# Optimization experiments

Measured on AMD Instinct MI355X. Metric: run time of the kernel, lower is better.

Reference implementation:

```python
import jax, jax.numpy as jnp
import numpy as np

B, LENGTH, D, IN = 32, 32, 384, 384
NCELLS = LENGTH * (LENGTH + 1) // 2  # 528

def _offsets():
    off = np.zeros(LENGTH, dtype=np.int64)
    for lvl in range(1, LENGTH):
        off[lvl] = off[lvl - 1] + (LENGTH - (lvl - 1))
    return off

_OFF = _offsets()

def _inside_index(level):
    Ls = LENGTH - level
    pos = np.arange(Ls)[:, None]
    k = np.arange(level)[None, :]
    left = _OFF[k] + pos                      # span (k, pos)
    right = _OFF[level - k - 1] + pos + k + 1  # span (level-k-1, pos+k+1)
    return jnp.asarray(left), jnp.asarray(right)

def _outside_index(level):
    Ls = LENGTH - level
    N = LENGTH - level - 1  # constant #contexts per position
    par = np.zeros((Ls, N), dtype=np.int64)
    sib = np.zeros((Ls, N), dtype=np.int64)
    for pos in range(Ls):
        j = 0
        for s in range(LENGTH - pos - level - 1):  # node is left child
            par[pos, j] = _OFF[level + s + 1] + pos
            sib[pos, j] = _OFF[s] + pos + level + 1
            j += 1
        for s in range(pos):  # node is right child
            par[pos, j] = _OFF[level + s + 1] + pos - s - 1
            sib[pos, j] = _OFF[s] + pos - s - 1
            j += 1
    return jnp.asarray(par), jnp.asarray(sib)

def sigma_h(x):
    return x * jnp.tanh(jnp.sqrt(jax.nn.sigmoid(x)))

def layer_norm(x, g, b, eps=1e-5):
    mu = x.mean(-1, keepdims=True)
    var = ((x - mu) ** 2).mean(-1, keepdims=True)
    return (x - mu) * jax.lax.rsqrt(var + eps) * g + b

def compose(l, r, W0, W1, B0, W2, B1):
    h = sigma_h(l @ W0 + r @ W1 + B0)
    return sigma_h(h @ W2 + B1)

def bilinear(u, v, M):
    return jnp.einsum('blnd,de,blne->bln', u, M, v)[..., None]

def setup_inputs() -> dict:
    key = jax.random.key(0)
    ks = jax.random.split(key, 16)
    sc = 1.0 / np.sqrt(D)
    mk = lambda k, shp: (jax.random.normal(k, shp, dtype=jnp.float32) * sc)
    inp = {
        'x': jax.random.normal(ks[0], (B, LENGTH, IN), dtype=jnp.float32),
        'leaf_W': mk(ks[1], (IN, D)), 'leaf_b': jnp.zeros((D,), jnp.float32),
        'in_ln_g': jnp.ones((D,), jnp.float32), 'in_ln_b': jnp.zeros((D,), jnp.float32),
        'out_ln_g': jnp.ones((D,), jnp.float32), 'out_ln_b': jnp.zeros((D,), jnp.float32),
        'root_h': jax.random.normal(ks[2], (D,), dtype=jnp.float32) * 0.02,
        'in_bi': mk(ks[3], (D, D)), 'out_bi': mk(ks[4], (D, D)),
        'in_W0': mk(ks[5], (D, D)), 'in_W1': mk(ks[6], (D, D)),
        'in_B0': jnp.zeros((D,), jnp.float32),
        'in_W2': mk(ks[7], (D, D)), 'in_B1': jnp.zeros((D,), jnp.float32),
        'out_W0': mk(ks[8], (D, D)), 'out_W1': mk(ks[9], (D, D)),
        'out_B0': jnp.zeros((D,), jnp.float32),
        'out_W2': mk(ks[10], (D, D)), 'out_B1': jnp.zeros((D,), jnp.float32),
    }
    return inp

def reference(x, leaf_W, leaf_b, in_ln_g, in_ln_b, out_ln_g, out_ln_b, root_h,
              in_bi, out_bi, in_W0, in_W1, in_B0, in_W2, in_B1,
              out_W0, out_W1, out_B0, out_W2, out_B1):
    # leaf transform
    h0 = layer_norm(sigma_h(x @ leaf_W + leaf_b), in_ln_g, in_ln_b)
    ih = jnp.zeros((B, NCELLS, D), x.dtype).at[:, :LENGTH].set(h0)
    is_ = jnp.zeros((B, NCELLS, 1), x.dtype)
    # inside pass (CKY chart, level-by-level)
    for level in range(1, LENGTH):
        li, ri = _inside_index(level)
        lh, rh = ih[:, li], ih[:, ri]   # [B, Ls, level, D]
        ls, rs = is_[:, li], is_[:, ri]
        sc = bilinear(lh, rh, in_bi) + ls + rs
        p = jax.nn.softmax(sc, axis=2)
        xc = compose(lh, rh, in_W0, in_W1, in_B0, in_W2, in_B1)
        hbar = layer_norm((p * xc).sum(2), in_ln_g, in_ln_b)
        sbar = (p * sc).sum(2)
        o = int(_OFF[level]); Ls = LENGTH - level
        ih = ih.at[:, o:o + Ls].set(hbar)
        is_ = is_.at[:, o:o + Ls].set(sbar)
    # outside pass
    oh = jnp.zeros((B, NCELLS, D), x.dtype)
    os_ = jnp.zeros((B, NCELLS, 1), x.dtype)
    root = layer_norm(jnp.broadcast_to(root_h, (B, 1, D)), out_ln_g, out_ln_b)
    oh = oh.at[:, -1:].set(root)
    for level in range(LENGTH - 2, -1, -1):
        pi, si = _outside_index(level)
        ph, sh = oh[:, pi], ih[:, si]   # parent outside / sibling inside
        ps, ss = os_[:, pi], is_[:, si]
        sc = bilinear(sh, ph, out_bi) + ss + ps
        p = jax.nn.softmax(sc, axis=2)
        xc = compose(ph, sh, out_W0, out_W1, out_B0, out_W2, out_B1)
        hbar = layer_norm((p * xc).sum(2), out_ln_g, out_ln_b)
        sbar = (p * sc).sum(2)
        o = int(_OFF[level]); Ls = LENGTH - level
        oh = oh.at[:, o:o + Ls].set(hbar)
        os_ = os_.at[:, o:o + Ls].set(sbar)
    return ih, is_, oh, os_
```

## Files before the change

### kernel.cpp

```cpp
#include <hip/hip_runtime.h>
#include <cstddef>

#define BDIM 32
#define LEN 32
#define DD 384
#define NCELLS 528

typedef _Float16 h16;
typedef __attribute__((ext_vector_type(8))) _Float16 v8h;
typedef __attribute__((ext_vector_type(4))) float v4f;

__device__ __forceinline__ int offf(int k) { return k * 32 - ((k * (k - 1)) >> 1); }
static inline int offh(int k) { return k * 32 - ((k * (k - 1)) >> 1); }

__device__ __forceinline__ float sigma_h_f(float x) {
  float s = 1.0f / (1.0f + __expf(-x));
  float r = sqrtf(s);
  float e2 = __expf(2.0f * r);
  float th = 1.0f - 2.0f / (e2 + 1.0f);
  return x * th;
}

__device__ __forceinline__ size_t rowbase(int r, int gLs, int gOff) {
  if (gLs == 0) return (size_t)r;
  int b = r / gLs;
  int p = r - b * gLs;
  return (size_t)b * NCELLS + gOff + p;
}

__device__ __forceinline__ void split16(float v, h16& h, h16& l) {
  h = (h16)v;
  l = (h16)(v - (float)h);
}

__global__ __launch_bounds__(256) void pack3_k(
    const float* __restrict__ w0, const float* __restrict__ w1,
    const float* __restrict__ bi, const float* __restrict__ ow1,
    const float* __restrict__ obi, const float* __restrict__ w2,
    const float* __restrict__ ow2, const float* __restrict__ ow0,
    const float* __restrict__ lw, const float* __restrict__ x,
    h16* __restrict__ WCth, h16* __restrict__ WCtl,
    h16* __restrict__ W2th, h16* __restrict__ W2tl,
    h16* __restrict__ OW2th, h16* __restrict__ OW2tl,
    h16* __restrict__ OW0th, h16* __restrict__ OW0tl,
    h16* __restrict__ LWth, h16* __restrict__ LWtl,
    h16* __restrict__ xh, h16* __restrict__ xl,
    float* __restrict__ isp, float* __restrict__ osp) {
  int i = blockIdx.x * 256 + threadIdx.x;
  if (i < 1920 * 384) {
    int n = i / 384, k = i - n * 384;
    int sel = n / 384, c = n - sel * 384;
    const float* src = sel == 0 ? w0 : sel == 1 ? w1 : sel == 2 ? bi
                       : sel == 3 ? ow1 : obi;
    float v = src[k * 384 + c];
    h16 h, l; split16(v, h, l);
    WCth[i] = h; WCtl[i] = l;
  }
  if (i < 384 * 384) {
    int n = i / 384, k = i - n * 384;
    h16 h, l;
    split16(w2[k * 384 + n], h, l);  W2th[i] = h;  W2tl[i] = l;
    split16(ow2[k * 384 + n], h, l); OW2th[i] = h; OW2tl[i] = l;
    split16(ow0[k * 384 + n], h, l); OW0th[i] = h; OW0tl[i] = l;
    split16(lw[k * 384 + n], h, l);  LWth[i] = h;  LWtl[i] = l;
  }
  if (i < 1024 * 384) {
    h16 h, l; split16(x[i], h, l);
    xh[i] = h; xl[i] = l;
  }
  if (i < BDIM * NCELLS) { isp[i] = 0.0f; osp[i] = 0.0f; }
}

__global__ __launch_bounds__(256) void gemmh(
    const h16* __restrict__ Ahp, const h16* __restrict__ Alp,
    const h16* __restrict__ Bth, const h16* __restrict__ Btl,
    const float* __restrict__ bias, float* __restrict__ C,
    int M, int N, int act, int gLs, int gOff) {
  __shared__ h16 Ah[64][40], Al[64][40];
  __shared__ h16 Bh[128][40], Bl[128][40];
  int tid = threadIdx.x;
  int w = tid >> 6, lane = tid & 63;
  int m0 = blockIdx.x * 64, n0 = blockIdx.y * 128;
  int r = lane & 15, q = lane >> 4;

  v4f acc[4][2];
#pragma unroll
  for (int i = 0; i < 4; ++i)
#pragma unroll
    for (int j = 0; j < 2; ++j) acc[i][j] = (v4f){0.f, 0.f, 0.f, 0.f};

  int sar = tid >> 2;
  int sak = (tid & 3) << 3;
  const h16* Aph = nullptr;
  const h16* Apl = nullptr;
  if (m0 + sar < M) {
    size_t rb = (size_t)(m0 + sar) * DD;
    Aph = Ahp + rb + sak;
    Apl = Alp + rb + sak;
  }
  int sbc = tid >> 1;
  int sbk = (tid & 1) << 4;
  const h16* Bph = Bth + (size_t)(n0 + sbc) * DD + sbk;
  const h16* Bpl = Btl + (size_t)(n0 + sbc) * DD + sbk;

  for (int k0 = 0; k0 < DD; k0 += 32) {
    v8h a_h = (v8h){0.f, 0.f, 0.f, 0.f, 0.f, 0.f, 0.f, 0.f};
    v8h a_l = a_h;
    if (Aph) {
      a_h = *reinterpret_cast<const v8h*>(Aph + k0);
      a_l = *reinterpret_cast<const v8h*>(Apl + k0);
    }
    v8h b_h0 = *reinterpret_cast<const v8h*>(Bph + k0);
    v8h b_h1 = *reinterpret_cast<const v8h*>(Bph + k0 + 8);
    v8h b_l0 = *reinterpret_cast<const v8h*>(Bpl + k0);
    v8h b_l1 = *reinterpret_cast<const v8h*>(Bpl + k0 + 8);
    __syncthreads();
    *reinterpret_cast<v8h*>(&Ah[sar][sak]) = a_h;
    *reinterpret_cast<v8h*>(&Al[sar][sak]) = a_l;
    *reinterpret_cast<v8h*>(&Bh[sbc][sbk]) = b_h0;
    *reinterpret_cast<v8h*>(&Bh[sbc][sbk + 8]) = b_h1;
    *reinterpret_cast<v8h*>(&Bl[sbc][sbk]) = b_l0;
    *reinterpret_cast<v8h*>(&Bl[sbc][sbk + 8]) = b_l1;
    __syncthreads();
    v8h afh[4], afl[4], bfh[2], bfl[2];
#pragma unroll
    for (int i = 0; i < 4; ++i) {
      afh[i] = *reinterpret_cast<const v8h*>(&Ah[i * 16 + r][q * 8]);
      afl[i] = *reinterpret_cast<const v8h*>(&Al[i * 16 + r][q * 8]);
    }
#pragma unroll
    for (int j = 0; j < 2; ++j) {
      bfh[j] = *reinterpret_cast<const v8h*>(&Bh[w * 32 + j * 16 + r][q * 8]);
      bfl[j] = *reinterpret_cast<const v8h*>(&Bl[w * 32 + j * 16 + r][q * 8]);
    }
#pragma unroll
    for (int i = 0; i < 4; ++i)
#pragma unroll
      for (int j = 0; j < 2; ++j) {
        acc[i][j] = __builtin_amdgcn_mfma_f32_16x16x32_f16(afl[i], bfh[j], acc[i][j], 0, 0, 0);
        acc[i][j] = __builtin_amdgcn_mfma_f32_16x16x32_f16(afh[i], bfl[j], acc[i][j], 0, 0, 0);
        acc[i][j] = __builtin_amdgcn_mfma_f32_16x16x32_f16(afh[i], bfh[j], acc[i][j], 0, 0, 0);
      }
  }

#pragma unroll
  for (int i = 0; i < 4; ++i) {
#pragma unroll
    for (int reg = 0; reg < 4; ++reg) {
      int rr = m0 + i * 16 + q * 4 + reg;
      if (rr >= M) continue;
      size_t cb = rowbase(rr, gLs, gOff) * (size_t)N;
#pragma unroll
      for (int j = 0; j < 2; ++j) {
        int col = n0 + w * 32 + j * 16 + r;
        float v = acc[i][j][reg];
        if (bias) v += bias[col];
        if (act) v = sigma_h_f(v);
        C[cb + col] = v;
      }
    }
  }
}

__global__ __launch_bounds__(256) void k1_in(
    const float* __restrict__ PC, const float* __restrict__ ihp,
    float* __restrict__ isp, h16* __restrict__ Hh, h16* __restrict__ Hl,
    float* __restrict__ Pw, const float* __restrict__ B0,
    int L, int Ls, int offL) {
  int g = blockIdx.x;
  int b = g / Ls, pos = g - b * Ls;
  int tid = threadIdx.x, lane = tid & 63, wv = tid >> 6;
  __shared__ float scs[32];
  size_t cb = (size_t)b * NCELLS;
  for (int n = wv; n < L; n += 4) {
    int lc = offf(n) + pos;
    int rc = offf(L - 1 - n) + pos + n + 1;
    const float* u = PC + (cb + lc) * 1920 + 768;
    const float* v = ihp + (cb + rc) * (size_t)DD;
    float s = 0.0f;
#pragma unroll
    for (int jj = 0; jj < 6; ++jj) s += u[lane + 64 * jj] * v[lane + 64 * jj];
#pragma unroll
    for (int o = 32; o; o >>= 1) s += __shfl_xor(s, o, 64);
    if (lane == 0) scs[n] = s + isp[cb + lc] + isp[cb + rc];
  }
  __syncthreads();
  if (wv == 0) {
    float v = (lane < L) ? scs[lane] : -3.0e38f;
    float m = v;
#pragma unroll
    for (int o = 32; o; o >>= 1) m = fmaxf(m, __shfl_xor(m, o, 64));
    float e = (lane < L) ? __expf(v - m) : 0.0f;
    float S = e;
#pragma unroll
    for (int o = 32; o; o >>= 1) S += __shfl_xor(S, o, 64);
    float pn = e / S;
    if (lane < L) Pw[(size_t)g * L + lane] = pn;
    float sb = (lane < L) ? pn * v : 0.0f;
#pragma unroll
    for (int o = 32; o; o >>= 1) sb += __shfl_xor(sb, o, 64);
    if (lane == 0) isp[cb + offL + pos] = sb;
  }
  for (int n = 0; n < L; ++n) {
    int lc = offf(n) + pos;
    int rc = offf(L - 1 - n) + pos + n + 1;
    const float* A0r = PC + (cb + lc) * 1920;
    const float* A1r = PC + (cb + rc) * 1920 + 384;
    size_t hb = ((size_t)g * L + n) * DD;
    for (int k = tid; k < DD; k += 256) {
      float v = sigma_h_f(A0r[k] + A1r[k] + B0[k]);
      h16 h = (h16)v;
      Hh[hb + k] = h;
      Hl[hb + k] = (h16)(v - (float)h);
    }
  }
}

__global__ __launch_bounds__(256) void k1_out(
    const float* __restrict__ PC, const float* __restrict__ P0,
    const float* __restrict__ ohp, const float* __restrict__ isp,
    float* __restrict__ osp, h16* __restrict__ Hh, h16* __restrict__ Hl,
    float* __restrict__ Pw, const float* __restrict__ B0,
    int L, int Ls, int Nc, int offL) {
  int g = blockIdx.x;
  int b = g / Ls, pos = g - b * Ls;
  int tid = threadIdx.x, lane = tid & 63, wv = tid >> 6;
  __shared__ float scs[32];
  size_t cb = (size_t)b * NCELLS;
  int cnt0 = 31 - pos - L;
  for (int j = wv; j < Nc; j += 4) {
    int par, sib;
    if (j < cnt0) { par = offf(L + j + 1) + pos; sib = offf(j) + pos + L + 1; }
    else { int s2 = j - cnt0; par = offf(L + s2 + 1) + pos - s2 - 1; sib = offf(s2) + pos - s2 - 1; }
    const float* u = PC + (cb + sib) * 1920 + 1536;
    const float* v = ohp + (cb + par) * (size_t)DD;
    float s = 0.0f;
#pragma unroll
    for (int jj = 0; jj < 6; ++jj) s += u[lane + 64 * jj] * v[lane + 64 * jj];
#pragma unroll
    for (int o = 32; o; o >>= 1) s += __shfl_xor(s, o, 64);
    if (lane == 0) scs[j] = s + isp[cb + sib] + osp[cb + par];
  }
  __syncthreads();
  if (wv == 0) {
    float v = (lane < Nc) ? scs[lane] : -3.0e38f;
    float m = v;
#pragma unroll
    for (int o = 32; o; o >>= 1) m = fmaxf(m, __shfl_xor(m, o, 64));
    float e = (lane < Nc) ? __expf(v - m) : 0.0f;
    float S = e;
#pragma unroll
    for (int o = 32; o; o >>= 1) S += __shfl_xor(S, o, 64);
    float pn = e / S;
    if (lane < Nc) Pw[(size_t)g * Nc + lane] = pn;
    float sb = (lane < Nc) ? pn * v : 0.0f;
#pragma unroll
    for (int o = 32; o; o >>= 1) sb += __shfl_xor(sb, o, 64);
    if (lane == 0) osp[cb + offL + pos] = sb;
  }
  for (int j = 0; j < Nc; ++j) {
    int par, sib;
    if (j < cnt0) { par = offf(L + j + 1) + pos; sib = offf(j) + pos + L + 1; }
    else { int s2 = j - cnt0; par = offf(L + s2 + 1) + pos - s2 - 1; sib = offf(s2) + pos - s2 - 1; }
    const float* p0r = P0 + (cb + par) * (size_t)DD;
    const float* s1r = PC + (cb + sib) * 1920 + 1152;
    size_t hb = ((size_t)g * Nc + j) * DD;
    for (int k = tid; k < DD; k += 256) {
      float v = sigma_h_f(p0r[k] + s1r[k] + B0[k]);
      h16 h = (h16)v;
      Hh[hb + k] = h;
      Hl[hb + k] = (h16)(v - (float)h);
    }
  }
}

__global__ __launch_bounds__(128) void k3_red_ln(
    const float* __restrict__ XC, const float* __restrict__ Pw,
    const float* __restrict__ lng, const float* __restrict__ lnb,
    float* __restrict__ outArr, h16* __restrict__ outh, h16* __restrict__ outl,
    int L, int Ls, int offL) {
  int g = blockIdx.x;
  int b = g / Ls, pos = g - b * Ls;
  int tid = threadIdx.x;
  float a0 = 0, a1 = 0, a2 = 0;
  const float* base = XC + (size_t)g * L * DD;
  for (int n = 0; n < L; ++n) {
    float pw = Pw ? Pw[(size_t)g * L + n] : 1.0f;
    const float* row = base + (size_t)n * DD;
    a0 += pw * row[tid];
    a1 += pw * row[tid + 128];
    a2 += pw * row[tid + 256];
  }
  int lane = tid & 63, wv = tid >> 6;
  float s = a0 + a1 + a2;
#pragma unroll
  for (int o = 32; o; o >>= 1) s += __shfl_xor(s, o, 64);
  __shared__ float r1[2], r2[2];
  if (lane == 0) r1[wv] = s;
  __syncthreads();
  float mean = (r1[0] + r1[1]) * (1.0f / 384.0f);
  float d0 = a0 - mean, d1 = a1 - mean, d2 = a2 - mean;
  float q = d0 * d0 + d1 * d1 + d2 * d2;
#pragma unroll
  for (int o = 32; o; o >>= 1) q += __shfl_xor(q, o, 64);
  if (lane == 0) r2[wv] = q;
  __syncthreads();
  float var = (r2[0] + r2[1]) * (1.0f / 384.0f);
  float inv = rsqrtf(var + 1e-5f);
  size_t ob = ((size_t)b * NCELLS + offL + pos) * DD;
  float* out = outArr + ob;
  float v0 = d0 * inv * lng[tid]       + lnb[tid];
  float v1 = d1 * inv * lng[tid + 128] + lnb[tid + 128];
  float v2 = d2 * inv * lng[tid + 256] + lnb[tid + 256];
  out[tid]       = v0;
  out[tid + 128] = v1;
  out[tid + 256] = v2;
  size_t sb = (size_t)g * DD;
  h16 h;
  h = (h16)v0; outh[sb + tid]       = h; outl[sb + tid]       = (h16)(v0 - (float)h);
  h = (h16)v1; outh[sb + tid + 128] = h; outl[sb + tid + 128] = (h16)(v1 - (float)h);
  h = (h16)v2; outh[sb + tid + 256] = h; outl[sb + tid + 256] = (h16)(v2 - (float)h);
}

__global__ __launch_bounds__(384) void root_k(
    const float* __restrict__ rooth, const float* __restrict__ lng,
    const float* __restrict__ lnb, const float* __restrict__ W0,
    float* __restrict__ ohp, float* __restrict__ P0) {
  int tid = threadIdx.x;
  int lane = tid & 63, wv = tid >> 6;
  __shared__ float rl[384];
  __shared__ float r1[6], r2[6];
  float x = rooth[tid];
  float s = x;
#pragma unroll
  for (int o = 32; o; o >>= 1) s += __shfl_xor(s, o, 64);
  if (lane == 0) r1[wv] = s;
  __syncthreads();
  float mean = (r1[0] + r1[1] + r1[2] + r1[3] + r1[4] + r1[5]) * (1.0f / 384.0f);
  float d = x - mean;
  float q = d * d;
#pragma unroll
  for (int o = 32; o; o >>= 1) q += __shfl_xor(q, o, 64);
  if (lane == 0) r2[wv] = q;
  __syncthreads();
  float var = (r2[0] + r2[1] + r2[2] + r2[3] + r2[4] + r2[5]) * (1.0f / 384.0f);
  float inv = rsqrtf(var + 1e-5f);
  float v = d * inv * lng[tid] + lnb[tid];
  rl[tid] = v;
  __syncthreads();
  for (int b2 = 0; b2 < BDIM; ++b2)
    ohp[((size_t)b2 * NCELLS + 527) * DD + tid] = v;
  float acc = 0.0f;
  for (int d2 = 0; d2 < 384; ++d2) acc += rl[d2] * W0[(size_t)d2 * 384 + tid];
  for (int b2 = 0; b2 < BDIM; ++b2)
    P0[((size_t)b2 * NCELLS + 527) * DD + tid] = acc;
}

extern "C" void kernel_launch(void* const* d_in, const int* in_sizes, int n_in,
                              void* d_out, int out_size, void* d_ws, size_t ws_size,
                              hipStream_t stream) {
  const float* x        = (const float*)d_in[0];
  const float* leaf_W   = (const float*)d_in[1];
  const float* leaf_b   = (const float*)d_in[2];
  const float* in_ln_g  = (const float*)d_in[3];
  const float* in_ln_b  = (const float*)d_in[4];
  const float* out_ln_g = (const float*)d_in[5];
  const float* out_ln_b = (const float*)d_in[6];
  const float* root_h   = (const float*)d_in[7];
  const float* in_bi    = (const float*)d_in[8];
  const float* out_bi   = (const float*)d_in[9];
  const float* in_W0    = (const float*)d_in[10];
  const float* in_W1    = (const float*)d_in[11];
  const float* in_B0    = (const float*)d_in[12];
  const float* in_W2    = (const float*)d_in[13];
  const float* in_B1    = (const float*)d_in[14];
  const float* out_W0   = (const float*)d_in[15];
  const float* out_W1   = (const float*)d_in[16];
  const float* out_B0   = (const float*)d_in[17];
  const float* out_W2   = (const float*)d_in[18];
  const float* out_B1   = (const float*)d_in[19];

  float* ih  = (float*)d_out;
  float* isp = ih + (size_t)BDIM * NCELLS * DD;
  float* oh  = isp + (size_t)BDIM * NCELLS;
  float* osp = oh + (size_t)BDIM * NCELLS * DD;

  float* PC  = (float*)d_ws;
  float* P0  = PC + (size_t)32440320;
  float* XCb = P0 + (size_t)6488064;
  float* Pw  = XCb + (size_t)12189696;
  h16* Hh    = (h16*)(Pw + 31744);
  h16* Hl    = Hh + (size_t)12189696;
  h16* WCth  = Hl + (size_t)12189696;
  h16* WCtl  = WCth + (size_t)737280;
  h16* W2th  = WCtl + (size_t)737280;
  h16* W2tl  = W2th + (size_t)147456;
  h16* OW2th = W2tl + (size_t)147456;
  h16* OW2tl = OW2th + (size_t)147456;
  h16* OW0th = OW2tl + (size_t)147456;
  h16* OW0tl = OW0th + (size_t)147456;
  h16* LWth  = OW0tl + (size_t)147456;
  h16* LWtl  = LWth + (size_t)147456;
  h16* xh = Hh;
  h16* xl = Hl;
  h16* Ch = Hh + (size_t)16384 * DD;
  h16* Cl = Hl + (size_t)16384 * DD;

  pack3_k<<<2880, 256, 0, stream>>>(in_W0, in_W1, in_bi, out_W1, out_bi,
                                    in_W2, out_W2, out_W0, leaf_W, x,
                                    WCth, WCtl, W2th, W2tl, OW2th, OW2tl,
                                    OW0th, OW0tl, LWth, LWtl, xh, xl,
                                    isp, osp);

  gemmh<<<dim3(16, 3), 256, 0, stream>>>(xh, xl, LWth, LWtl, leaf_b, XCb, 1024, 384, 1, 0, 0);
  k3_red_ln<<<1024, 128, 0, stream>>>(XCb, nullptr, in_ln_g, in_ln_b, ih, Ch, Cl, 1, 32, 0);
  gemmh<<<dim3(16, 15), 256, 0, stream>>>(Ch, Cl, WCth, WCtl, nullptr, PC, 1024, 1920, 0, 32, 0);

  for (int L = 1; L < LEN; ++L) {
    int Ls = LEN - L, G = BDIM * Ls, M = G * L, off = offh(L);
    k1_in<<<G, 256, 0, stream>>>(PC, ih, isp, Hh, Hl, Pw, in_B0, L, Ls, off);
    gemmh<<<dim3((M + 63) / 64, 3), 256, 0, stream>>>(Hh, Hl, W2th, W2tl, in_B1, XCb, M, 384, 1, 0, 0);
    k3_red_ln<<<G, 128, 0, stream>>>(XCb, Pw, in_ln_g, in_ln_b, ih, Ch, Cl, L, Ls, off);
    gemmh<<<dim3((G + 63) / 64, 15), 256, 0, stream>>>(Ch, Cl, WCth, WCtl, nullptr, PC, G, 1920, 0, Ls, off);
  }

  root_k<<<1, 384, 0, stream>>>(root_h, out_ln_g, out_ln_b, out_W0, oh, P0);

  for (int L = LEN - 2; L >= 0; --L) {
    int Ls = LEN - L, Nc = LEN - 1 - L, G = BDIM * Ls, M = G * Nc, off = offh(L);
    k1_out<<<G, 256, 0, stream>>>(PC, P0, oh, isp, osp, Hh, Hl, Pw, out_B0, L, Ls, Nc, off);
    gemmh<<<dim3((M + 63) / 64, 3), 256, 0, stream>>>(Hh, Hl, OW2th, OW2tl, out_B1, XCb, M, 384, 1, 0, 0);
    k3_red_ln<<<G, 128, 0, stream>>>(XCb, Pw, out_ln_g, out_ln_b, oh, Ch, Cl, Nc, Ls, off);
    if (L > 0)
      gemmh<<<dim3((G + 63) / 64, 3), 256, 0, stream>>>(Ch, Cl, OW0th, OW0tl, nullptr, P0, G, 384, 0, Ls, off);
  }
}
```

Before: 4.927 ms.

## Fuse per-level scoring, compose GEMM, weighted reduction and layernorm into one kernel

Replaces the per-level sequence k1 (score+softmax+first sigma_h) → W2 GEMM → reduction+layernorm with a single templated kernel. It computes the scores and softmax, builds the hidden activation on the fly in LDS, runs the split-fp16 MFMA against W2, and accumulates the softmax-weighted sums in shared memory with LDS atomics before the layernorm. This removes the large H and XC intermediate round trips through global memory and two launches per level. In exchange, each block holds only a few cells, so the W2 weights are re-streamed per block and grids get small at deep levels (T capped by G/256), which risks low occupancy and heavy LDS use.

Result: slower. 5.718 ms (+16.1%).

```diff
diff --git a/kernel.cpp b/kernel.cpp
--- a/kernel.cpp
+++ b/kernel.cpp
@@ -31,6 +31,22 @@
 __device__ __forceinline__ void split16(float v, h16& h, h16& l) {
   h = (h16)v;
   l = (h16)(v - (float)h);
+}
+
+__device__ __forceinline__ void pairidx(int inside, int lvl, int np, int pos,
+                                        int n, int& uC, int& vC, int& aC,
+                                        int& bC) {
+  if (inside) {
+    int lc = offf(n) + pos;
+    int rc = offf(np - 1 - n) + pos + n + 1;
+    uC = lc; vC = rc; aC = lc; bC = rc;
+  } else {
+    int par, sib;
+    int cnt0 = 31 - pos - lvl;
+    if (n < cnt0) { par = offf(lvl + n + 1) + pos; sib = offf(n) + pos + lvl + 1; }
+    else { int s2 = n - cnt0; par = offf(lvl + s2 + 1) + pos - s2 - 1; sib = offf(s2) + pos - s2 - 1; }
+    uC = sib; vC = par; aC = par; bC = sib;
+  }
 }
 
 __global__ __launch_bounds__(256) void pack3_k(
@@ -162,115 +178,211 @@
   }
 }
 
-__global__ __launch_bounds__(256) void k1_in(
-    const float* __restrict__ PC, const float* __restrict__ ihp,
-    float* __restrict__ isp, h16* __restrict__ Hh, h16* __restrict__ Hl,
-    float* __restrict__ Pw, const float* __restrict__ B0,
-    int L, int Ls, int offL) {
-  int g = blockIdx.x;
-  int b = g / Ls, pos = g - b * Ls;
+template <int MT>
+__global__ __launch_bounds__(256) void lvl_k(
+    const float* __restrict__ PC, const float* __restrict__ P0,
+    const float* __restrict__ vArr, const float* __restrict__ sX,
+    float* __restrict__ sY, float* __restrict__ outF32,
+    h16* __restrict__ Ch, h16* __restrict__ Cl,
+    const h16* __restrict__ Wth, const h16* __restrict__ Wtl,
+    const float* __restrict__ B0, const float* __restrict__ B1,
+    const float* __restrict__ lng, const float* __restrict__ lnb,
+    int lvl, int np, int Ls, int offL, int T, int inside) {
+  __shared__ h16 Ah[64][36], Al[64][36];
+  __shared__ h16 Bh[384][36], Bl[384][36];
+  __shared__ float b0s[384], b1s[384];
+  __shared__ float scb[4][32], pb[4][32];
+  __shared__ float hs[4][388];
+  __shared__ float r1[4], r2[4];
+
   int tid = threadIdx.x, lane = tid & 63, wv = tid >> 6;
-  __shared__ float scs[32];
-  size_t cb = (size_t)b * NCELLS;
-  for (int n = wv; n < L; n += 4) {
-    int lc = offf(n) + pos;
-    int rc = offf(L - 1 - n) + pos + n + 1;
-    const float* u = PC + (cb + lc) * 1920 + 768;
-    const float* v = ihp + (cb + rc) * (size_t)DD;
-    float s = 0.0f;
-#pragma unroll
-    for (int jj = 0; jj < 6; ++jj) s += u[lane + 64 * jj] * v[lane + 64 * jj];
-#pragma unroll
-    for (int o = 32; o; o >>= 1) s += __shfl_xor(s, o, 64);
-    if (lane == 0) scs[n] = s + isp[cb + lc] + isp[cb + rc];
-  }
-  __syncthreads();
-  if (wv == 0) {
-    float v = (lane < L) ? scs[lane] : -3.0e38f;
+  int G = BDIM * Ls;
+  int g0 = blockIdx.x * T;
+  int M_tile = T * np;
+
+  for (int k = tid; k < 384; k += 256) { b0s[k] = B0[k]; b1s[k] = B1[k]; }
+  for (int k = tid; k < 4 * 388; k += 256) (&hs[0][0])[k] = 0.0f;
+
+  for (int d = wv; d < M_tile; d += 4) {
+    int c = d / np, n = d - c * np;
+    int g = g0 + c;
+    if (g < G) {
+      int b = g / Ls, pos = g - b * Ls;
+      size_t cb = (size_t)b * NCELLS;
+      int uC, vC, aC, bC;
+      pairidx(inside, lvl, np, pos, n, uC, vC, aC, bC);
+      const float* u = PC + (cb + uC) * 1920 + (inside ? 768 : 1536);
+      const float* v = vArr + (cb + vC) * (size_t)DD;
+      float s = 0.0f;
+#pragma unroll
+      for (int jj = 0; jj < 6; ++jj) s += u[lane + 64 * jj] * v[lane + 64 * jj];
+#pragma unroll
+      for (int o = 32; o; o >>= 1) s += __shfl_xor(s, o, 64);
+      if (lane == 0)
+        scb[c][n] = s + sX[cb + (inside ? aC : bC)] + sY[cb + (inside ? bC : aC)];
+    }
+  }
+  __syncthreads();
+  for (int c = wv; c < T; c += 4) {
+    int g = g0 + c;
+    float v = (lane < np && g < G) ? scb[c][lane] : -3.0e38f;
     float m = v;
 #pragma unroll
     for (int o = 32; o; o >>= 1) m = fmaxf(m, __shfl_xor(m, o, 64));
-    float e = (lane < L) ? __expf(v - m) : 0.0f;
+    float e = (lane < np) ? __expf(v - m) : 0.0f;
     float S = e;
 #pragma unroll
     for (int o = 32; o; o >>= 1) S += __shfl_xor(S, o, 64);
     float pn = e / S;
-    if (lane < L) Pw[(size_t)g * L + lane] = pn;
-    float sb = (lane < L) ? pn * v : 0.0f;
+    if (lane < np) pb[c][lane] = pn;
+    float sb = (lane < np) ? pn * v : 0.0f;
 #pragma unroll
     for (int o = 32; o; o >>= 1) sb += __shfl_xor(sb, o, 64);
-    if (lane == 0) isp[cb + offL + pos] = sb;
-  }
-  for (int n = 0; n < L; ++n) {
-    int lc = offf(n) + pos;
-    int rc = offf(L - 1 - n) + pos + n + 1;
-    const float* A0r = PC + (cb + lc) * 1920;
-    const float* A1r = PC + (cb + rc) * 1920 + 384;
-    size_t hb = ((size_t)g * L + n) * DD;
-    for (int k = tid; k < DD; k += 256) {
-      float v = sigma_h_f(A0r[k] + A1r[k] + B0[k]);
-      h16 h = (h16)v;
-      Hh[hb + k] = h;
-      Hl[hb + k] = (h16)(v - (float)h);
-    }
-  }
-}
-
-__global__ __launch_bounds__(256) void k1_out(
-    const float* __restrict__ PC, const float* __restrict__ P0,
-    const float* __restrict__ ohp, const float* __restrict__ isp,
-    float* __restrict__ osp, h16* __restrict__ Hh, h16* __restrict__ Hl,
-    float* __restrict__ Pw, const float* __restrict__ B0,
-    int L, int Ls, int Nc, int offL) {
-  int g = blockIdx.x;
-  int b = g / Ls, pos = g - b * Ls;
-  int tid = threadIdx.x, lane = tid & 63, wv = tid >> 6;
-  __shared__ float scs[32];
-  size_t cb = (size_t)b * NCELLS;
-  int cnt0 = 31 - pos - L;
-  for (int j = wv; j < Nc; j += 4) {
-    int par, sib;
-    if (j < cnt0) { par = offf(L + j + 1) + pos; sib = offf(j) + pos + L + 1; }
-    else { int s2 = j - cnt0; par = offf(L + s2 + 1) + pos - s2 - 1; sib = offf(s2) + pos - s2 - 1; }
-    const float* u = PC + (cb + sib) * 1920 + 1536;
-    const float* v = ohp + (cb + par) * (size_t)DD;
-    float s = 0.0f;
-#pragma unroll
-    for (int jj = 0; jj < 6; ++jj) s += u[lane + 64 * jj] * v[lane + 64 * jj];
+    if (lane == 0 && g < G) {
+      int b = g / Ls, pos = g - b * Ls;
+      sY[(size_t)b * NCELLS + offL + pos] = sb;
+    }
+  }
+
+  int r = lane & 15, q = lane >> 4;
+  int sar = tid >> 2;
+  int sak = (tid & 3) << 3;
+  const float* A0p = nullptr;
+  const float* A1p = nullptr;
+  if (sar < M_tile) {
+    int c = sar / np, n = sar - c * np;
+    int g = g0 + c;
+    if (g < G) {
+      int b = g / Ls, pos = g - b * Ls;
+      size_t cb = (size_t)b * NCELLS;
+      int uC, vC, aC, bC;
+      pairidx(inside, lvl, np, pos, n, uC, vC, aC, bC);
+      A0p = (inside ? PC + (cb + aC) * 1920 : P0 + (cb + aC) * (size_t)DD) + sak;
+      A1p = PC + (cb + bC) * 1920 + (inside ? 384 : 1152) + sak;
+    }
+  }
+
+  v4f acc[MT][6];
+#pragma unroll
+  for (int i = 0; i < MT; ++i)
+#pragma unroll
+    for (int j = 0; j < 6; ++j) acc[i][j] = (v4f){0.f, 0.f, 0.f, 0.f};
+
+  for (int k0 = 0; k0 < DD; k0 += 32) {
+    float4 x0, x1, y0, y1;
+    if (A0p) {
+      x0 = *reinterpret_cast<const float4*>(A0p + k0);
+      x1 = *reinterpret_cast<const float4*>(A0p + k0 + 4);
+      y0 = *reinterpret_cast<const float4*>(A1p + k0);
+      y1 = *reinterpret_cast<const float4*>(A1p + k0 + 4);
+    }
+    v8h bh_[6], bl_[6];
+#pragma unroll
+    for (int i2 = 0; i2 < 6; ++i2) {
+      int p = tid + 256 * i2;
+      int col = p >> 2, ch = (p & 3) << 3;
+      bh_[i2] = *reinterpret_cast<const v8h*>(Wth + (size_t)col * DD + k0 + ch);
+      bl_[i2] = *reinterpret_cast<const v8h*>(Wtl + (size_t)col * DD + k0 + ch);
+    }
+    __syncthreads();
+    {
+      v8h hi = (v8h){0.f,0.f,0.f,0.f,0.f,0.f,0.f,0.f}, lo = hi;
+      if (A0p) {
+        float av[8] = {x0.x, x0.y, x0.z, x0.w, x1.x, x1.y, x1.z, x1.w};
+        float bv[8] = {y0.x, y0.y, y0.z, y0.w, y1.x, y1.y, y1.z, y1.w};
+#pragma unroll
+        for (int t = 0; t < 8; ++t) {
+          float hv = sigma_h_f(av[t] + bv[t] + b0s[k0 + sak + t]);
+          h16 h = (h16)hv;
+          hi[t] = h;
+          lo[t] = (h16)(hv - (float)h);
+        }
+      }
+      *reinterpret_cast<v8h*>(&Ah[sar][sak]) = hi;
+      *reinterpret_cast<v8h*>(&Al[sar][sak]) = lo;
+    }
+#pragma unroll
+    for (int i2 = 0; i2 < 6; ++i2) {
+      int p = tid + 256 * i2;
+      int col = p >> 2, ch = (p & 3) << 3;
+      *reinterpret_cast<v8h*>(&Bh[col][ch]) = bh_[i2];
+      *reinterpret_cast<v8h*>(&Bl[col][ch]) = bl_[i2];
+    }
+    __syncthreads();
+    v8h afh[MT], afl[MT];
+#pragma unroll
+    for (int i = 0; i < MT; ++i) {
+      afh[i] = *reinterpret_cast<const v8h*>(&Ah[i * 16 + r][q * 8]);
+      afl[i] = *reinterpret_cast<const v8h*>(&Al[i * 16 + r][q * 8]);
+    }
+#pragma unroll
+    for (int j = 0; j < 6; ++j) {
+      v8h bfh = *reinterpret_cast<const v8h*>(&Bh[wv * 96 + j * 16 + r][q * 8]);
+      v8h bfl = *reinterpret_cast<const v8h*>(&Bl[wv * 96 + j * 16 + r][q * 8]);
+#pragma unroll
+      for (int i = 0; i < MT; ++i) {
+        acc[i][j] = __builtin_amdgcn_mfma_f32_16x16x32_f16(afl[i], bfh, acc[i][j], 0, 0, 0);
+        acc[i][j] = __builtin_amdgcn_mfma_f32_16x16x32_f16(afh[i], bfl, acc[i][j], 0, 0, 0);
+        acc[i][j] = __builtin_amdgcn_mfma_f32_16x16x32_f16(afh[i], bfh, acc[i][j], 0, 0, 0);
+      }
+    }
+  }
+
+#pragma unroll
+  for (int i = 0; i < MT; ++i) {
+#pragma unroll
+    for (int j = 0; j < 6; ++j) {
+      int col = wv * 96 + j * 16 + r;
+#pragma unroll
+      for (int reg = 0; reg < 4; ++reg) {
+        int row = i * 16 + q * 4 + reg;
+        if (row < M_tile) {
+          int c = row / np, n = row - c * np;
+          float xc = sigma_h_f(acc[i][j][reg] + b1s[col]);
+          atomicAdd(&hs[c][col], pb[c][n] * xc);
+        }
+      }
+    }
+  }
+  __syncthreads();
+
+  for (int c0 = 0; c0 < T; c0 += 2) {
+    int gi = tid >> 7;
+    int c = c0 + gi;
+    int t2 = tid & 127;
+    float e0 = 0.f, e1 = 0.f, e2 = 0.f;
+    if (c < T) { e0 = hs[c][t2]; e1 = hs[c][t2 + 128]; e2 = hs[c][t2 + 256]; }
+    float s = e0 + e1 + e2;
 #pragma unroll
     for (int o = 32; o; o >>= 1) s += __shfl_xor(s, o, 64);
-    if (lane == 0) scs[j] = s + isp[cb + sib] + osp[cb + par];
-  }
-  __syncthreads();
-  if (wv == 0) {
-    float v = (lane < Nc) ? scs[lane] : -3.0e38f;
-    float m = v;
-#pragma unroll
-    for (int o = 32; o; o >>= 1) m = fmaxf(m, __shfl_xor(m, o, 64));
-    float e = (lane < Nc) ? __expf(v - m) : 0.0f;
-    float S = e;
-#pragma unroll
-    for (int o = 32; o; o >>= 1) S += __shfl_xor(S, o, 64);
-    float pn = e / S;
-    if (lane < Nc) Pw[(size_t)g * Nc + lane] = pn;
-    float sb = (lane < Nc) ? pn * v : 0.0f;
-#pragma unroll
-    for (int o = 32; o; o >>= 1) sb += __shfl_xor(sb, o, 64);
-    if (lane == 0) osp[cb + offL + pos] = sb;
-  }
-  for (int j = 0; j < Nc; ++j) {
-    int par, sib;
-    if (j < cnt0) { par = offf(L + j + 1) + pos; sib = offf(j) + pos + L + 1; }
-    else { int s2 = j - cnt0; par = offf(L + s2 + 1) + pos - s2 - 1; sib = offf(s2) + pos - s2 - 1; }
-    const float* p0r = P0 + (cb + par) * (size_t)DD;
-    const float* s1r = PC + (cb + sib) * 1920 + 1152;
-    size_t hb = ((size_t)g * Nc + j) * DD;
-    for (int k = tid; k < DD; k += 256) {
-      float v = sigma_h_f(p0r[k] + s1r[k] + B0[k]);
-      h16 h = (h16)v;
-      Hh[hb + k] = h;
-      Hl[hb + k] = (h16)(v - (float)h);
-    }
+    if (lane == 0) r1[wv] = s;
+    __syncthreads();
+    float mean = (r1[gi * 2] + r1[gi * 2 + 1]) * (1.0f / 384.0f);
+    float d0 = e0 - mean, d1 = e1 - mean, d2 = e2 - mean;
+    float qq = d0 * d0 + d1 * d1 + d2 * d2;
+#pragma unroll
+    for (int o = 32; o; o >>= 1) qq += __shfl_xor(qq, o, 64);
+    if (lane == 0) r2[wv] = qq;
+    __syncthreads();
+    float var = (r2[gi * 2] + r2[gi * 2 + 1]) * (1.0f / 384.0f);
+    float inv = rsqrtf(var + 1e-5f);
+    int g = g0 + c;
+    if (c < T && g < G) {
+      int b = g / Ls, pos = g - b * Ls;
+      size_t ob = ((size_t)b * NCELLS + offL + pos) * (size_t)DD;
+      float v0 = d0 * inv * lng[t2]       + lnb[t2];
+      float v1 = d1 * inv * lng[t2 + 128] + lnb[t2 + 128];
+      float v2 = d2 * inv * lng[t2 + 256] + lnb[t2 + 256];
+      outF32[ob + t2]       = v0;
+      outF32[ob + t2 + 128] = v1;
+      outF32[ob + t2 + 256] = v2;
+      size_t sb2 = (size_t)g * DD;
+      h16 h;
+      h = (h16)v0; Ch[sb2 + t2]       = h; Cl[sb2 + t2]       = (h16)(v0 - (float)h);
+      h = (h16)v1; Ch[sb2 + t2 + 128] = h; Cl[sb2 + t2 + 128] = (h16)(v1 - (float)h);
+      h = (h16)v2; Ch[sb2 + t2 + 256] = h; Cl[sb2 + t2 + 256] = (h16)(v2 - (float)h);
+    }
+    __syncthreads();
   }
 }
 
@@ -354,6 +466,21 @@
   for (int d2 = 0; d2 < 384; ++d2) acc += rl[d2] * W0[(size_t)d2 * 384 + tid];
   for (int b2 = 0; b2 < BDIM; ++b2)
     P0[((size_t)b2 * NCELLS + 527) * DD + tid] = acc;
+}
+
+static void launch_lvl(int nb, hipStream_t stream, int mt,
+                       const float* PC, const float* P0, const float* vArr,
+                       const float* sX, float* sY, float* outF32,
+                       h16* Ch, h16* Cl, const h16* Wth, const h16* Wtl,
+                       const float* B0, const float* B1,
+                       const float* lng, const float* lnb,
+                       int lvl, int np, int Ls, int offL, int T, int inside) {
+  switch (mt) {
+    case 1: lvl_k<1><<<nb, 256, 0, stream>>>(PC, P0, vArr, sX, sY, outF32, Ch, Cl, Wth, Wtl, B0, B1, lng, lnb, lvl, np, Ls, offL, T, inside); break;
+    case 2: lvl_k<2><<<nb, 256, 0, stream>>>(PC, P0, vArr, sX, sY, outF32, Ch, Cl, Wth, Wtl, B0, B1, lng, lnb, lvl, np, Ls, offL, T, inside); break;
+    case 3: lvl_k<3><<<nb, 256, 0, stream>>>(PC, P0, vArr, sX, sY, outF32, Ch, Cl, Wth, Wtl, B0, B1, lng, lnb, lvl, np, Ls, offL, T, inside); break;
+    default: lvl_k<4><<<nb, 256, 0, stream>>>(PC, P0, vArr, sX, sY, outF32, Ch, Cl, Wth, Wtl, B0, B1, lng, lnb, lvl, np, Ls, offL, T, inside); break;
+  }
 }
 
 extern "C" void kernel_launch(void* const* d_in, const int* in_sizes, int n_in,
@@ -406,6 +533,8 @@
   h16* Ch = Hh + (size_t)16384 * DD;
   h16* Cl = Hl + (size_t)16384 * DD;
 
+  (void)Pw;
+
   pack3_k<<<2880, 256, 0, stream>>>(in_W0, in_W1, in_bi, out_W1, out_bi,
                                     in_W2, out_W2, out_W0, leaf_W, x,
                                     WCth, WCtl, W2th, W2tl, OW2th, OW2tl,
@@ -417,20 +546,32 @@
   gemmh<<<dim3(16, 15), 256, 0, stream>>>(Ch, Cl, WCth, WCtl, nullptr, PC, 1024, 1920, 0, 32, 0);
 
   for (int L = 1; L < LEN; ++L) {
-    int Ls = LEN - L, G = BDIM * Ls, M = G * L, off = offh(L);
-    k1_in<<<G, 256, 0, stream>>>(PC, ih, isp, Hh, Hl, Pw, in_B0, L, Ls, off);
-    gemmh<<<dim3((M + 63) / 64, 3), 256, 0, stream>>>(Hh, Hl, W2th, W2tl, in_B1, XCb, M, 384, 1, 0, 0);
-    k3_red_ln<<<G, 128, 0, stream>>>(XCb, Pw, in_ln_g, in_ln_b, ih, Ch, Cl, L, Ls, off);
+    int Ls = LEN - L, G = BDIM * Ls, off = offh(L);
+    int T = 64 / L;
+    int cap = (G + 255) / 256;
+    if (T > cap) T = cap;
+    if (T > 4) T = 4;
+    if (T < 1) T = 1;
+    int nb = (G + T - 1) / T;
+    int mt = (T * L + 15) >> 4;
+    launch_lvl(nb, stream, mt, PC, nullptr, ih, isp, isp, ih, Ch, Cl,
+               W2th, W2tl, in_B0, in_B1, in_ln_g, in_ln_b, L, L, Ls, off, T, 1);
     gemmh<<<dim3((G + 63) / 64, 15), 256, 0, stream>>>(Ch, Cl, WCth, WCtl, nullptr, PC, G, 1920, 0, Ls, off);
   }
 
   root_k<<<1, 384, 0, stream>>>(root_h, out_ln_g, out_ln_b, out_W0, oh, P0);
 
   for (int L = LEN - 2; L >= 0; --L) {
-    int Ls = LEN - L, Nc = LEN - 1 - L, G = BDIM * Ls, M = G * Nc, off = offh(L);
-    k1_out<<<G, 256, 0, stream>>>(PC, P0, oh, isp, osp, Hh, Hl, Pw, out_B0, L, Ls, Nc, off);
-    gemmh<<<dim3((M + 63) / 64, 3), 256, 0, stream>>>(Hh, Hl, OW2th, OW2tl, out_B1, XCb, M, 384, 1, 0, 0);
-    k3_red_ln<<<G, 128, 0, stream>>>(XCb, Pw, out_ln_g, out_ln_b, oh, Ch, Cl, Nc, Ls, off);
+    int Ls = LEN - L, G = BDIM * Ls, Nc = LEN - 1 - L, off = offh(L);
+    int T = 64 / Nc;
+    int cap = (G + 255) / 256;
+    if (T > cap) T = cap;
+    if (T > 4) T = 4;
+    if (T < 1) T = 1;
+    int nb = (G + T - 1) / T;
+    int mt = (T * Nc + 15) >> 4;
+    launch_lvl(nb, stream, mt, PC, P0, oh, isp, osp, oh, Ch, Cl,
+               OW2th, OW2tl, out_B0, out_B1, out_ln_g, out_ln_b, L, Nc, Ls, off, T, 0);
     if (L > 0)
       gemmh<<<dim3((G + 63) / 64, 3), 256, 0, stream>>>(Ch, Cl, OW0th, OW0tl, nullptr, P0, G, 384, 0, Ls, off);
   }
```

## Fuse softmax-weighted reduction into GEMM epilogue via atomics and merge hidden compute

Applied to the files above, without the earlier changes.

The second compose GEMM now applies bias and sigma_h, multiplies by the softmax weight, and atomically accumulates into a per-span hbar buffer. This removes the full XC intermediate write and the reduction pass in the layer-norm kernel, which now only normalizes. The first-layer compose activation is moved into the score loop of k1_in/k1_out, with the bias cached in shared memory and hbar zeroed there. This adds float atomic contention and makes the summation order nondeterministic.

After: 6.410 ms. +30.1%, slower.

```diff
diff --git a/kernel.cpp b/kernel.cpp
--- a/kernel.cpp
+++ b/kernel.cpp
@@ -75,7 +75,8 @@
     const h16* __restrict__ Ahp, const h16* __restrict__ Alp,
     const h16* __restrict__ Bth, const h16* __restrict__ Btl,
     const float* __restrict__ bias, float* __restrict__ C,
-    int M, int N, int act, int gLs, int gOff) {
+    float* __restrict__ hbar, const float* __restrict__ Pw,
+    int M, int N, int act, int np, int gLs, int gOff) {
   __shared__ h16 Ah[64][40], Al[64][40];
   __shared__ h16 Bh[128][40], Bl[128][40];
   int tid = threadIdx.x;
@@ -143,6 +144,29 @@
       }
   }
 
+  if (hbar) {
+#pragma unroll
+    for (int i = 0; i < 4; ++i) {
+#pragma unroll
+      for (int reg = 0; reg < 4; ++reg) {
+        int rr = m0 + i * 16 + q * 4 + reg;
+        if (rr >= M) continue;
+#pragma unroll
+        for (int j = 0; j < 2; ++j) {
+          int col = n0 + w * 32 + j * 16 + r;
+          float v = sigma_h_f(acc[i][j][reg] + bias[col]);
+          if (np == 1) {
+            hbar[(size_t)rr * DD + col] = v;
+          } else {
+            float pw = Pw[rr];
+            atomicAdd(&hbar[(size_t)(rr / np) * DD + col], pw * v);
+          }
+        }
+      }
+    }
+    return;
+  }
+
 #pragma unroll
   for (int i = 0; i < 4; ++i) {
 #pragma unroll
@@ -166,12 +190,18 @@
     const float* __restrict__ PC, const float* __restrict__ ihp,
     float* __restrict__ isp, h16* __restrict__ Hh, h16* __restrict__ Hl,
     float* __restrict__ Pw, const float* __restrict__ B0,
-    int L, int Ls, int offL) {
+    float* __restrict__ hbar, int L, int Ls, int offL) {
   int g = blockIdx.x;
   int b = g / Ls, pos = g - b * Ls;
   int tid = threadIdx.x, lane = tid & 63, wv = tid >> 6;
   __shared__ float scs[32];
+  __shared__ float b0s[384];
   size_t cb = (size_t)b * NCELLS;
+  for (int k = tid; k < 384; k += 256) {
+    b0s[k] = B0[k];
+    hbar[(size_t)g * DD + k] = 0.0f;
+  }
+  __syncthreads();
   for (int n = wv; n < L; n += 4) {
     int lc = offf(n) + pos;
     int rc = offf(L - 1 - n) + pos + n + 1;
@@ -183,6 +213,17 @@
 #pragma unroll
     for (int o = 32; o; o >>= 1) s += __shfl_xor(s, o, 64);
     if (lane == 0) scs[n] = s + isp[cb + lc] + isp[cb + rc];
+    const float* A0r = PC + (cb + lc) * 1920;
+    const float* A1r = PC + (cb + rc) * 1920 + 384;
+    size_t hb = ((size_t)g * L + n) * DD;
+#pragma unroll
+    for (int jj = 0; jj < 6; ++jj) {
+      int k = lane + 64 * jj;
+      float hv = sigma_h_f(A0r[k] + A1r[k] + b0s[k]);
+      h16 h = (h16)hv;
+      Hh[hb + k] = h;
+      Hl[hb + k] = (h16)(hv - (float)h);
+    }
   }
   __syncthreads();
   if (wv == 0) {
@@ -200,19 +241,6 @@
 #pragma unroll
     for (int o = 32; o; o >>= 1) sb += __shfl_xor(sb, o, 64);
     if (lane == 0) isp[cb + offL + pos] = sb;
-  }
-  for (int n = 0; n < L; ++n) {
-    int lc = offf(n) + pos;
-    int rc = offf(L - 1 - n) + pos + n + 1;
-    const float* A0r = PC + (cb + lc) * 1920;
-    const float* A1r = PC + (cb + rc) * 1920 + 384;
-    size_t hb = ((size_t)g * L + n) * DD;
-    for (int k = tid; k < DD; k += 256) {
-      float v = sigma_h_f(A0r[k] + A1r[k] + B0[k]);
-      h16 h = (h16)v;
-      Hh[hb + k] = h;
-      Hl[hb + k] = (h16)(v - (float)h);
-    }
   }
 }
 
@@ -221,13 +249,19 @@
     const float* __restrict__ ohp, const float* __restrict__ isp,
     float* __restrict__ osp, h16* __restrict__ Hh, h16* __restrict__ Hl,
     float* __restrict__ Pw, const float* __restrict__ B0,
-    int L, int Ls, int Nc, int offL) {
+    float* __restrict__ hbar, int L, int Ls, int Nc, int offL) {
   int g = blockIdx.x;
   int b = g / Ls, pos = g - b * Ls;
   int tid = threadIdx.x, lane = tid & 63, wv = tid >> 6;
   __shared__ float scs[32];
+  __shared__ float b0s[384];
   size_t cb = (size_t)b * NCELLS;
   int cnt0 = 31 - pos - L;
+  for (int k = tid; k < 384; k += 256) {
+    b0s[k] = B0[k];
+    hbar[(size_t)g * DD + k] = 0.0f;
+  }
+  __syncthreads();
   for (int j = wv; j < Nc; j += 4) {
     int par, sib;
     if (j < cnt0) { par = offf(L + j + 1) + pos; sib = offf(j) + pos + L + 1; }
@@ -240,6 +274,17 @@
 #pragma unroll
     for (int o = 32; o; o >>= 1) s += __shfl_xor(s, o, 64);
     if (lane == 0) scs[j] = s + isp[cb + sib] + osp[cb + par];
+    const float* p0r = P0 + (cb + par) * (size_t)DD;
+    const float* s1r = PC + (cb + sib) * 1920 + 1152;
+    size_t hb = ((size_t)g * Nc + j) * DD;
+#pragma unroll
+    for (int jj = 0; jj < 6; ++jj) {
+      int k = lane + 64 * jj;
+      float hv = sigma_h_f(p0r[k] + s1r[k] + b0s[k]);
+      h16 h = (h16)hv;
+      Hh[hb + k] = h;
+      Hl[hb + k] = (h16)(hv - (float)h);
+    }
   }
   __syncthreads();
   if (wv == 0) {
@@ -258,39 +303,18 @@
     for (int o = 32; o; o >>= 1) sb += __shfl_xor(sb, o, 64);
     if (lane == 0) osp[cb + offL + pos] = sb;
   }
-  for (int j = 0; j < Nc; ++j) {
-    int par, sib;
-    if (j < cnt0) { par = offf(L + j + 1) + pos; sib = offf(j) + pos + L + 1; }
-    else { int s2 = j - cnt0; par = offf(L + s2 + 1) + pos - s2 - 1; sib = offf(s2) + pos - s2 - 1; }
-    const float* p0r = P0 + (cb + par) * (size_t)DD;
-    const float* s1r = PC + (cb + sib) * 1920 + 1152;
-    size_t hb = ((size_t)g * Nc + j) * DD;
-    for (int k = tid; k < DD; k += 256) {
-      float v = sigma_h_f(p0r[k] + s1r[k] + B0[k]);
-      h16 h = (h16)v;
-      Hh[hb + k] = h;
-      Hl[hb + k] = (h16)(v - (float)h);
-    }
-  }
-}
-
-__global__ __launch_bounds__(128) void k3_red_ln(
-    const float* __restrict__ XC, const float* __restrict__ Pw,
+}
+
+__global__ __launch_bounds__(128) void k3_ln(
+    const float* __restrict__ hbar,
     const float* __restrict__ lng, const float* __restrict__ lnb,
     float* __restrict__ outArr, h16* __restrict__ outh, h16* __restrict__ outl,
-    int L, int Ls, int offL) {
+    int Ls, int offL) {
   int g = blockIdx.x;
   int b = g / Ls, pos = g - b * Ls;
   int tid = threadIdx.x;
-  float a0 = 0, a1 = 0, a2 = 0;
-  const float* base = XC + (size_t)g * L * DD;
-  for (int n = 0; n < L; ++n) {
-    float pw = Pw ? Pw[(size_t)g * L + n] : 1.0f;
-    const float* row = base + (size_t)n * DD;
-    a0 += pw * row[tid];
-    a1 += pw * row[tid + 128];
-    a2 += pw * row[tid + 256];
-  }
+  const float* hrow = hbar + (size_t)g * DD;
+  float a0 = hrow[tid], a1 = hrow[tid + 128], a2 = hrow[tid + 256];
   int lane = tid & 63, wv = tid >> 6;
   float s = a0 + a1 + a2;
 #pragma unroll
@@ -405,6 +429,7 @@
   h16* xl = Hl;
   h16* Ch = Hh + (size_t)16384 * DD;
   h16* Cl = Hl + (size_t)16384 * DD;
+  float* hbar = XCb;
 
   pack3_k<<<2880, 256, 0, stream>>>(in_W0, in_W1, in_bi, out_W1, out_bi,
                                     in_W2, out_W2, out_W0, leaf_W, x,
@@ -412,26 +437,32 @@
                                     OW0th, OW0tl, LWth, LWtl, xh, xl,
                                     isp, osp);
 
-  gemmh<<<dim3(16, 3), 256, 0, stream>>>(xh, xl, LWth, LWtl, leaf_b, XCb, 1024, 384, 1, 0, 0);
-  k3_red_ln<<<1024, 128, 0, stream>>>(XCb, nullptr, in_ln_g, in_ln_b, ih, Ch, Cl, 1, 32, 0);
-  gemmh<<<dim3(16, 15), 256, 0, stream>>>(Ch, Cl, WCth, WCtl, nullptr, PC, 1024, 1920, 0, 32, 0);
+  gemmh<<<dim3(16, 3), 256, 0, stream>>>(xh, xl, LWth, LWtl, leaf_b, nullptr,
+                                         hbar, nullptr, 1024, 384, 1, 1, 0, 0);
+  k3_ln<<<1024, 128, 0, stream>>>(hbar, in_ln_g, in_ln_b, ih, Ch, Cl, 32, 0);
+  gemmh<<<dim3(16, 15), 256, 0, stream>>>(Ch, Cl, WCth, WCtl, nullptr, PC,
+                                          nullptr, nullptr, 1024, 1920, 0, 1, 32, 0);
 
   for (int L = 1; L < LEN; ++L) {
     int Ls = LEN - L, G = BDIM * Ls, M = G * L, off = offh(L);
-    k1_in<<<G, 256, 0, stream>>>(PC, ih, isp, Hh, Hl, Pw, in_B0, L, Ls, off);
-    gemmh<<<dim3((M + 63) / 64, 3), 256, 0, stream>>>(Hh, Hl, W2th, W2tl, in_B1, XCb, M, 384, 1, 0, 0);
-    k3_red_ln<<<G, 128, 0, stream>>>(XCb, Pw, in_ln_g, in_ln_b, ih, Ch, Cl, L, Ls, off);
-    gemmh<<<dim3((G + 63) / 64, 15), 256, 0, stream>>>(Ch, Cl, WCth, WCtl, nullptr, PC, G, 1920, 0, Ls, off);
+    k1_in<<<G, 256, 0, stream>>>(PC, ih, isp, Hh, Hl, Pw, in_B0, hbar, L, Ls, off);
+    gemmh<<<dim3((M + 63) / 64, 3), 256, 0, stream>>>(Hh, Hl, W2th, W2tl, in_B1,
+                                                      nullptr, hbar, Pw, M, 384, 1, L, 0, 0);
+    k3_ln<<<G, 128, 0, stream>>>(hbar, in_ln_g, in_ln_b, ih, Ch, Cl, Ls, off);
+    gemmh<<<dim3((G + 63) / 64, 15), 256, 0, stream>>>(Ch, Cl, WCth, WCtl, nullptr, PC,
+                                                       nullptr, nullptr, G, 1920, 0, 1, Ls, off);
   }
 
   root_k<<<1, 384, 0, stream>>>(root_h, out_ln_g, out_ln_b, out_W0, oh, P0);
 
   for (int L = LEN - 2; L >= 0; --L) {
-    int Ls = LEN - L, Nc = LEN - 1 - L, G = BDIM * Ls, M = G * Nc, off = offh(L);
-    k1_out<<<G, 256, 0, stream>>>(PC, P0, oh, isp, osp, Hh, Hl, Pw, out_B0, L, Ls, Nc, off);
-    gemmh<<<dim3((M + 63) / 64, 3), 256, 0, stream>>>(Hh, Hl, OW2th, OW2tl, out_B1, XCb, M, 384, 1, 0, 0);
-    k3_red_ln<<<G, 128, 0, stream>>>(XCb, Pw, out_ln_g, out_ln_b, oh, Ch, Cl, Nc, Ls, off);
+    int Ls = LEN - L, G = BDIM * Ls, Nc = LEN - 1 - L, M = G * Nc, off = offh(L);
+    k1_out<<<G, 256, 0, stream>>>(PC, P0, oh, isp, osp, Hh, Hl, Pw, out_B0, hbar, L, Ls, Nc, off);
+    gemmh<<<dim3((M + 63) / 64, 3), 256, 0, stream>>>(Hh, Hl, OW2th, OW2tl, out_B1,
+                                                      nullptr, hbar, Pw, M, 384, 1, Nc, 0, 0);
+    k3_ln<<<G, 128, 0, stream>>>(hbar, out_ln_g, out_ln_b, oh, Ch, Cl, Ls, off);
     if (L > 0)
-      gemmh<<<dim3((G + 63) / 64, 3), 256, 0, stream>>>(Ch, Cl, OW0th, OW0tl, nullptr, P0, G, 384, 0, Ls, off);
-  }
-}
+      gemmh<<<dim3((G + 63) / 64, 3), 256, 0, stream>>>(Ch, Cl, OW0th, OW0tl, nullptr, P0,
+                                                        nullptr, nullptr, G, 384, 0, 1, Ls, off);
+  }
+}
```
